# Kernel tuning notes

Measured on AMD Instinct MI355X. Metric: run time of the kernel, lower is better.

## Reference

```python
import jax, jax.numpy as jnp
import numpy as np

N = 524288          # query points
N_COMP = 36         # sdf_n_comp
GRID = 512          # cubic grid resolution
SDF_DIM = 256
APP_DIM = 128
MAT_MODE = [(0, 1), (0, 2), (1, 2)]
VEC_MODE = [2, 1, 0]
PE_FREQS = (1.0, 2.0, 4.0)  # sdf_multires=3, log-sampled 2^0..2^2


def _pos_enc(x):
    # NeRF embedder, include_input=True: [x, sin(f x), cos(f x) per freq]
    outs = [x]
    for f in PE_FREQS:
        outs.append(jnp.sin(x * f))
        outs.append(jnp.cos(x * f))
    return jnp.concatenate(outs, axis=-1)  # (N, 21)


def _bilinear_plane(plane, gx, gy):
    # plane: (C, H, W); gx indexes W, gy indexes H; align_corners=True
    C, H, W = plane.shape
    px = (gx + 1.0) * 0.5 * (W - 1)
    py = (gy + 1.0) * 0.5 * (H - 1)
    x0 = jnp.clip(jnp.floor(px), 0, W - 2).astype(jnp.int32)
    y0 = jnp.clip(jnp.floor(py), 0, H - 2).astype(jnp.int32)
    x1, y1 = x0 + 1, y0 + 1
    wx = px - x0
    wy = py - y0
    f00 = plane[:, y0, x0]  # (C, N)
    f01 = plane[:, y0, x1]
    f10 = plane[:, y1, x0]
    f11 = plane[:, y1, x1]
    return (f00 * (1 - wx) + f01 * wx) * (1 - wy) + (f10 * (1 - wx) + f11 * wx) * wy


def _linear_line(line, g):
    # line: (C, L); g in [-1, 1]; align_corners=True
    C, L = line.shape
    p = (g + 1.0) * 0.5 * (L - 1)
    i0 = jnp.clip(jnp.floor(p), 0, L - 2).astype(jnp.int32)
    w = p - i0
    return line[:, i0] * (1 - w) + line[:, i0 + 1] * w  # (C, N)


def setup_inputs() -> dict:
    key = jax.random.key(0)
    ks = jax.random.split(key, 6)
    xyz = jax.random.uniform(ks[0], (N, 3), dtype=jnp.float32)  # points in aabb [0,1]^3
    planes = jax.random.normal(ks[1], (3, N_COMP, GRID, GRID), dtype=jnp.float32) * 0.1
    lines = jax.random.normal(ks[2], (3, N_COMP, GRID), dtype=jnp.float32) * 0.1
    in_ch = N_COMP * 3 + 21  # 129
    W1 = jax.random.normal(ks[3], (in_ch, SDF_DIM), dtype=jnp.float32) * (np.sqrt(2.0) / np.sqrt(SDF_DIM))
    b1 = jnp.zeros((SDF_DIM,), dtype=jnp.float32)
    W2 = jax.random.normal(ks[4], (SDF_DIM, 1 + APP_DIM), dtype=jnp.float32) * 0.0001 + np.sqrt(np.pi) / np.sqrt(SDF_DIM)
    b2 = jnp.full((1 + APP_DIM,), -0.2, dtype=jnp.float32)  # init_radius bias
    return {"xyz": xyz, "planes": planes, "lines": lines, "W1": W1, "b1": b1, "W2": W2, "b2": b2}


def reference(xyz, planes, lines, W1, b1, W2, b2):
    # contraction: normalize aabb [0,1]^3 -> [-1,1]
    xn = 2.0 * xyz - 1.0  # (N, 3)
    # sampling coords are detached in the original (coordinate_plane.detach())
    xs = jax.lax.stop_gradient(xn)
    feats = []
    for i in range(3):
        m0, m1 = MAT_MODE[i]
        pfeat = _bilinear_plane(planes[i], xs[:, m0], xs[:, m1])  # (C, N)
        lfeat = _linear_line(lines[i], xs[:, VEC_MODE[i]])        # (C, N)
        feats.append(pfeat * lfeat)
    feat = jnp.concatenate(feats, axis=0).T  # (N, 3C)
    pe = _pos_enc(xn)                         # (N, 21)
    h = jnp.concatenate([feat, pe], axis=-1)  # (N, 129)
    h = jax.nn.softplus(100.0 * (h @ W1 + b1)) / 100.0  # Softplus(beta=100)
    out = h @ W2 + b2  # (N, 1 + app_dim); out[..., :1] is the SDF
    return out
```

## Files before the change

kernel.cpp:

```cpp
#include <hip/hip_runtime.h>
#include <math.h>

typedef unsigned short u16;
typedef unsigned int u32;
typedef __attribute__((ext_vector_type(8))) short short8;
typedef __attribute__((ext_vector_type(4))) float f32x4;

#define OFF_LINES_T 62914560u
#define OFF_W1S     63037440u
#define OFF_W2S     63119360u
#define WS_NEEDED   63217664u

__device__ __forceinline__ float bf_lo(u32 u){ union{u32 i;float f;} v; v.i = u << 16; return v.f; }
__device__ __forceinline__ float bf_hi(u32 u){ union{u32 i;float f;} v; v.i = u & 0xffff0000u; return v.f; }
__device__ __forceinline__ u16 f2bf(float f){ union{float f;u32 i;} v; v.f=f; u32 i=v.i; return (u16)((i + 0x7fffu + ((i>>16)&1u)) >> 16); }
__device__ __forceinline__ u32 pack2bf(float lo, float hi){ return (u32)f2bf(lo) | ((u32)f2bf(hi)<<16); }

__global__ void k_tp(const float* __restrict__ planes, u16* __restrict__ pt){
  int t = blockIdx.x*256 + threadIdx.x;
  int i = t >> 18;
  int yx = t & 262143;
  const float* src = planes + (size_t)i*9437184 + yx;
  uint4* dst = reinterpret_cast<uint4*>(pt + (size_t)t*40);
#pragma unroll
  for (int cc=0; cc<5; cc++){
    float v[8];
#pragma unroll
    for (int e=0;e<8;e++){
      int c = cc*8+e;
      v[e] = (c<36) ? src[(size_t)c*262144] : 0.f;
    }
    uint4 o; o.x=pack2bf(v[0],v[1]); o.y=pack2bf(v[2],v[3]); o.z=pack2bf(v[4],v[5]); o.w=pack2bf(v[6],v[7]);
    dst[cc]=o;
  }
}

__global__ void k_tl(const float* __restrict__ lines, u16* __restrict__ lt){
  int t = blockIdx.x*256 + threadIdx.x;
  int i = t >> 9, g = t & 511;
  const float* src = lines + (size_t)i*18432 + g;
  uint4* dst = reinterpret_cast<uint4*>(lt + (size_t)t*40);
#pragma unroll
  for (int cc=0; cc<5; cc++){
    float v[8];
#pragma unroll
    for (int e=0;e<8;e++){
      int c = cc*8+e;
      v[e] = (c<36) ? src[(size_t)c*512] : 0.f;
    }
    uint4 o; o.x=pack2bf(v[0],v[1]); o.y=pack2bf(v[2],v[3]); o.z=pack2bf(v[4],v[5]); o.w=pack2bf(v[6],v[7]);
    dst[cc]=o;
  }
}

__device__ __forceinline__ int map_k1(int kp){
  if (kp < 120){ int q = kp/40, r = kp - q*40; return (r<36) ? q*36 + r : -1; }
  if (kp < 141) return kp - 12;
  return -1;
}

__global__ void k_w1(const float* __restrict__ W1, u16* __restrict__ w1s){
  int t = blockIdx.x*256 + threadIdx.x;
  int lane = t & 63;
  int fid = t >> 6;
  int nt = fid/5, kt = fid - nt*5;
  int n = nt*16 + (lane & 15);
  int kb = kt*32 + (lane >> 4)*8;
  float v[8];
#pragma unroll
  for (int j=0;j<8;j++){ int k = map_k1(kb+j); v[j] = (k>=0) ? W1[k*256+n] : 0.f; }
  uint4 o; o.x=pack2bf(v[0],v[1]); o.y=pack2bf(v[2],v[3]); o.z=pack2bf(v[4],v[5]); o.w=pack2bf(v[6],v[7]);
  *reinterpret_cast<uint4*>(w1s + (size_t)t*8) = o;
}

__global__ void k_w2(const float* __restrict__ W2, u16* __restrict__ w2s){
  int t = blockIdx.x*256 + threadIdx.x;
  int lane = t & 63;
  int fid = t >> 6;
  int kb = (fid & 7)*32 + (lane >> 4)*8;
  int n = (fid >> 3)*16 + (lane & 15);
  float v[8];
#pragma unroll
  for (int j=0;j<8;j++){ int k = kb+j; v[j] = (n<129) ? W2[k*129+n] : 0.f; }
  uint4 o; o.x=pack2bf(v[0],v[1]); o.y=pack2bf(v[2],v[3]); o.z=pack2bf(v[4],v[5]); o.w=pack2bf(v[6],v[7]);
  *reinterpret_cast<uint4*>(w2s + (size_t)t*8) = o;
}

__device__ __forceinline__ u32 blend(u32 u00,u32 u01,u32 u10,u32 u11,u32 g0,u32 g1,
                                     float wx,float wy,float wz){
  float r[2];
#pragma unroll
  for (int h=0; h<2; h++){
    float f00 = h ? bf_hi(u00) : bf_lo(u00);
    float f01 = h ? bf_hi(u01) : bf_lo(u01);
    float f10 = h ? bf_hi(u10) : bf_lo(u10);
    float f11 = h ? bf_hi(u11) : bf_lo(u11);
    float e0  = h ? bf_hi(g0)  : bf_lo(g0);
    float e1  = h ? bf_hi(g1)  : bf_lo(g1);
    float a  = f00 + (f01-f00)*wx;
    float b  = f10 + (f11-f10)*wx;
    float pf = a + (b-a)*wy;
    float lf = e0 + (e1-e0)*wz;
    r[h] = pf*lf;
  }
  return pack2bf(r[0], r[1]);
}

#define FSTRIDE 168
#define HSTRIDE 264

__global__ void __launch_bounds__(256) k_main(
    const float* __restrict__ xyz, const u16* __restrict__ pt,
    const u16* __restrict__ lt, const u16* __restrict__ w1s,
    const u16* __restrict__ w2s, const float* __restrict__ b1,
    const float* __restrict__ b2, float* __restrict__ out)
{
  __shared__ u16 smem[64*HSTRIDE];
  const int tid = threadIdx.x;
  const int p = tid >> 2, q = tid & 3;
  const int gp = blockIdx.x*64 + p;
  const float u0 = xyz[gp*3], u1 = xyz[gp*3+1], u2 = xyz[gp*3+2];
  const float xn0 = 2.f*u0-1.f, xn1 = 2.f*u1-1.f, xn2 = 2.f*u2-1.f;

  if (q < 3){
    float gxv, gyv, gzv;
    if      (q==0){ gxv=xn0; gyv=xn1; gzv=xn2; }
    else if (q==1){ gxv=xn0; gyv=xn2; gzv=xn1; }
    else          { gxv=xn1; gyv=xn2; gzv=xn0; }
    float px=(gxv+1.0f)*0.5f*511.0f, py=(gyv+1.0f)*0.5f*511.0f, pz=(gzv+1.0f)*0.5f*511.0f;
    float fx=fminf(fmaxf(floorf(px),0.f),510.f);
    float fy=fminf(fmaxf(floorf(py),0.f),510.f);
    float fz=fminf(fmaxf(floorf(pz),0.f),510.f);
    int ix=(int)fx, iy=(int)fy, iz=(int)fz;
    float wx=px-fx, wy=py-fy, wz=pz-fz;
    const u16* base  = pt + (size_t)((q<<18)+(iy<<9)+ix)*40;
    const u16* lbase = lt + (size_t)((q<<9)+iz)*40;
    u16* dst = smem + p*FSTRIDE + q*40;
#pragma unroll
    for (int cc=0; cc<5; cc++){
      const uint4 a00 = *reinterpret_cast<const uint4*>(base + cc*8);
      const uint4 a01 = *reinterpret_cast<const uint4*>(base + 40 + cc*8);
      const uint4 a10 = *reinterpret_cast<const uint4*>(base + 20480 + cc*8);
      const uint4 a11 = *reinterpret_cast<const uint4*>(base + 20520 + cc*8);
      const uint4 e0  = *reinterpret_cast<const uint4*>(lbase + cc*8);
      const uint4 e1  = *reinterpret_cast<const uint4*>(lbase + 40 + cc*8);
      uint4 o;
      o.x = blend(a00.x,a01.x,a10.x,a11.x,e0.x,e1.x,wx,wy,wz);
      o.y = blend(a00.y,a01.y,a10.y,a11.y,e0.y,e1.y,wx,wy,wz);
      o.z = blend(a00.z,a01.z,a10.z,a11.z,e0.z,e1.z,wx,wy,wz);
      o.w = blend(a00.w,a01.w,a10.w,a11.w,e0.w,e1.w,wx,wy,wz);
      *reinterpret_cast<uint4*>(dst + cc*8) = o;
    }
  } else {
    float v[21];
    v[0]=xn0; v[1]=xn1; v[2]=xn2;
    v[3]=__sinf(xn0);      v[4]=__sinf(xn1);      v[5]=__sinf(xn2);
    v[6]=__cosf(xn0);      v[7]=__cosf(xn1);      v[8]=__cosf(xn2);
    v[9]=__sinf(2.f*xn0);  v[10]=__sinf(2.f*xn1); v[11]=__sinf(2.f*xn2);
    v[12]=__cosf(2.f*xn0); v[13]=__cosf(2.f*xn1); v[14]=__cosf(2.f*xn2);
    v[15]=__sinf(4.f*xn0); v[16]=__sinf(4.f*xn1); v[17]=__sinf(4.f*xn2);
    v[18]=__cosf(4.f*xn0); v[19]=__cosf(4.f*xn1); v[20]=__cosf(4.f*xn2);
    u16* dst = smem + p*FSTRIDE + 120;
#pragma unroll
    for (int cc=0; cc<5; cc++){
      float w0 = (cc*8+0<21)?v[cc*8+0]:0.f; float w1v=(cc*8+1<21)?v[cc*8+1]:0.f;
      float w2v= (cc*8+2<21)?v[cc*8+2]:0.f; float w3 =(cc*8+3<21)?v[cc*8+3]:0.f;
      float w4 = (cc*8+4<21)?v[cc*8+4]:0.f; float w5 =(cc*8+5<21)?v[cc*8+5]:0.f;
      float w6 = (cc*8+6<21)?v[cc*8+6]:0.f; float w7 =(cc*8+7<21)?v[cc*8+7]:0.f;
      uint4 o; o.x=pack2bf(w0,w1v); o.y=pack2bf(w2v,w3); o.z=pack2bf(w4,w5); o.w=pack2bf(w6,w7);
      *reinterpret_cast<uint4*>(dst + cc*8) = o;
    }
  }
  __syncthreads();

  const int lane = tid & 63;
  const int w = tid >> 6;
  const int lm = lane & 15;
  const int quad = lane >> 4;
  const f32x4 zero = {0.f,0.f,0.f,0.f};
  f32x4 acc1[4][4];
#pragma unroll
  for (int mt=0; mt<4; mt++)
#pragma unroll
    for (int nt=0; nt<4; nt++) acc1[mt][nt] = zero;

#pragma unroll
  for (int kt=0; kt<5; kt++){
    short8 a[4];
#pragma unroll
    for (int mt=0; mt<4; mt++)
      a[mt] = *reinterpret_cast<const short8*>(smem + (mt*16 + lm)*FSTRIDE + kt*32 + quad*8);
    short8 b[4];
#pragma unroll
    for (int nt=0; nt<4; nt++)
      b[nt] = *reinterpret_cast<const short8*>(w1s + (size_t)(((w*4+nt)*5 + kt)*64 + lane)*8);
#pragma unroll
    for (int mt=0; mt<4; mt++)
#pragma unroll
      for (int nt=0; nt<4; nt++)
        acc1[mt][nt] = __builtin_amdgcn_mfma_f32_16x16x32_bf16(a[mt], b[nt], acc1[mt][nt], 0,0,0);
  }
  __syncthreads();

#pragma unroll
  for (int nt=0; nt<4; nt++){
    int col = w*64 + nt*16 + lm;
    float bias = b1[col];
#pragma unroll
    for (int mt=0; mt<4; mt++){
#pragma unroll
      for (int r=0; r<4; r++){
        float xv = acc1[mt][nt][r] + bias;
        float z = 100.f*xv;
        float y = (z > 15.f) ? xv : __logf(1.f + __expf(z))*0.01f;
        int row = mt*16 + quad*4 + r;
        smem[row*HSTRIDE + col] = f2bf(y);
      }
    }
  }
  __syncthreads();

  f32x4 acc2[4][3];
#pragma unroll
  for (int mt=0; mt<4; mt++)
#pragma unroll
    for (int nt=0; nt<3; nt++) acc2[mt][nt] = zero;

#pragma unroll
  for (int kt=0; kt<8; kt++){
    short8 a[4];
#pragma unroll
    for (int mt=0; mt<4; mt++)
      a[mt] = *reinterpret_cast<const short8*>(smem + (mt*16 + lm)*HSTRIDE + kt*32 + quad*8);
    short8 b[3];
#pragma unroll
    for (int nt=0; nt<3; nt++){
      int ntg = w + nt*4;
      b[nt] = *reinterpret_cast<const short8*>(w2s + (size_t)((ntg*8 + kt)*64 + lane)*8);
    }
#pragma unroll
    for (int mt=0; mt<4; mt++)
#pragma unroll
      for (int nt=0; nt<3; nt++)
        acc2[mt][nt] = __builtin_amdgcn_mfma_f32_16x16x32_bf16(a[mt], b[nt], acc2[mt][nt], 0,0,0);
  }

#pragma unroll
  for (int nt=0; nt<3; nt++){
    int j = (w + nt*4)*16 + lm;
    if (j < 129){
      float bias = b2[j];
#pragma unroll
      for (int mt=0; mt<4; mt++){
#pragma unroll
        for (int r=0; r<4; r++){
          int row = mt*16 + quad*4 + r;
          out[(size_t)(blockIdx.x*64 + row)*129 + j] = acc2[mt][nt][r] + bias;
        }
      }
    }
  }
}

extern "C" void kernel_launch(void* const* d_in, const int* in_sizes, int n_in,
                              void* d_out, int out_size, void* d_ws, size_t ws_size,
                              hipStream_t stream) {
  const float* xyz    = (const float*)d_in[0];
  const float* planes = (const float*)d_in[1];
  const float* lines  = (const float*)d_in[2];
  const float* W1     = (const float*)d_in[3];
  const float* b1     = (const float*)d_in[4];
  const float* W2     = (const float*)d_in[5];
  const float* b2     = (const float*)d_in[6];
  if (ws_size < (size_t)WS_NEEDED) return;

  u16* pt  = (u16*)((char*)d_ws);
  u16* lt  = (u16*)((char*)d_ws + OFF_LINES_T);
  u16* w1s = (u16*)((char*)d_ws + OFF_W1S);
  u16* w2s = (u16*)((char*)d_ws + OFF_W2S);

  k_tp<<<3072, 256, 0, stream>>>(planes, pt);
  k_tl<<<6,    256, 0, stream>>>(lines,  lt);
  k_w1<<<20,   256, 0, stream>>>(W1, w1s);
  k_w2<<<24,   256, 0, stream>>>(W2, w2s);
  k_main<<<8192, 256, 0, stream>>>(xyz, pt, lt, w1s, w2s, b1, b2, (float*)d_out);
}
```

Before: 689.5 us.

## Double threads per block, split gather and MLP tiles across eight waves

k_main now runs 512 threads per block. Two threads share each plane's gather for a point, each taking half of the 40 channels with 8-byte loads, and the 8 waves split the MLP into 2 M-halves by 4 N-groups. Bf16 packing in the hot paths switches to a cheaper round-half-up conversion built on a byte-permute. The goal is more memory-level parallelism for the random gathers and lower per-thread register pressure, at the cost of narrower loads, redundant B-fragment loads across waves, and slightly different rounding.

```diff
diff --git a/kernel.cpp b/kernel.cpp
--- a/kernel.cpp
+++ b/kernel.cpp
@@ -3,6 +3,7 @@
 
 typedef unsigned short u16;
 typedef unsigned int u32;
+typedef __attribute__((ext_vector_type(2))) u32 u32x2;
 typedef __attribute__((ext_vector_type(8))) short short8;
 typedef __attribute__((ext_vector_type(4))) float f32x4;
 
@@ -15,6 +16,11 @@
 __device__ __forceinline__ float bf_hi(u32 u){ union{u32 i;float f;} v; v.i = u & 0xffff0000u; return v.f; }
 __device__ __forceinline__ u16 f2bf(float f){ union{float f;u32 i;} v; v.f=f; u32 i=v.i; return (u16)((i + 0x7fffu + ((i>>16)&1u)) >> 16); }
 __device__ __forceinline__ u32 pack2bf(float lo, float hi){ return (u32)f2bf(lo) | ((u32)f2bf(hi)<<16); }
+__device__ __forceinline__ u32 pack2bf_fast(float lo, float hi){
+  return __builtin_amdgcn_perm(__float_as_uint(hi) + 0x8000u,
+                               __float_as_uint(lo) + 0x8000u, 0x07060302u);
+}
+__device__ __forceinline__ u16 f2bf_fast(float f){ return (u16)((__float_as_uint(f) + 0x8000u) >> 16); }
 
 __global__ void k_tp(const float* __restrict__ planes, u16* __restrict__ pt){
   int t = blockIdx.x*256 + threadIdx.x;
@@ -54,7 +60,7 @@
 }
 
 __device__ __forceinline__ int map_k1(int kp){
-  if (kp < 120){ int q = kp/40, r = kp - q*40; return (r<36) ? q*36 + r : -1; }
+  if (kp < 120){ int g = kp/40, r = kp - g*40; return (r<36) ? g*36 + r : -1; }
   if (kp < 141) return kp - 12;
   return -1;
 }
@@ -103,13 +109,13 @@
     float lf = e0 + (e1-e0)*wz;
     r[h] = pf*lf;
   }
-  return pack2bf(r[0], r[1]);
+  return pack2bf_fast(r[0], r[1]);
 }
 
 #define FSTRIDE 168
 #define HSTRIDE 264
 
-__global__ void __launch_bounds__(256) k_main(
+__global__ void __launch_bounds__(512, 4) k_main(
     const float* __restrict__ xyz, const u16* __restrict__ pt,
     const u16* __restrict__ lt, const u16* __restrict__ w1s,
     const u16* __restrict__ w2s, const float* __restrict__ b1,
@@ -117,15 +123,16 @@
 {
   __shared__ u16 smem[64*HSTRIDE];
   const int tid = threadIdx.x;
-  const int p = tid >> 2, q = tid & 3;
+  const int p = tid >> 3, q = tid & 7;
   const int gp = blockIdx.x*64 + p;
   const float u0 = xyz[gp*3], u1 = xyz[gp*3+1], u2 = xyz[gp*3+2];
   const float xn0 = 2.f*u0-1.f, xn1 = 2.f*u1-1.f, xn2 = 2.f*u2-1.f;
 
-  if (q < 3){
+  if (q < 6){
+    const int i = q >> 1, part = q & 1;
     float gxv, gyv, gzv;
-    if      (q==0){ gxv=xn0; gyv=xn1; gzv=xn2; }
-    else if (q==1){ gxv=xn0; gyv=xn2; gzv=xn1; }
+    if      (i==0){ gxv=xn0; gyv=xn1; gzv=xn2; }
+    else if (i==1){ gxv=xn0; gyv=xn2; gzv=xn1; }
     else          { gxv=xn1; gyv=xn2; gzv=xn0; }
     float px=(gxv+1.0f)*0.5f*511.0f, py=(gyv+1.0f)*0.5f*511.0f, pz=(gzv+1.0f)*0.5f*511.0f;
     float fx=fminf(fmaxf(floorf(px),0.f),510.f);
@@ -133,25 +140,23 @@
     float fz=fminf(fmaxf(floorf(pz),0.f),510.f);
     int ix=(int)fx, iy=(int)fy, iz=(int)fz;
     float wx=px-fx, wy=py-fy, wz=pz-fz;
-    const u16* base  = pt + (size_t)((q<<18)+(iy<<9)+ix)*40;
-    const u16* lbase = lt + (size_t)((q<<9)+iz)*40;
-    u16* dst = smem + p*FSTRIDE + q*40;
-#pragma unroll
-    for (int cc=0; cc<5; cc++){
-      const uint4 a00 = *reinterpret_cast<const uint4*>(base + cc*8);
-      const uint4 a01 = *reinterpret_cast<const uint4*>(base + 40 + cc*8);
-      const uint4 a10 = *reinterpret_cast<const uint4*>(base + 20480 + cc*8);
-      const uint4 a11 = *reinterpret_cast<const uint4*>(base + 20520 + cc*8);
-      const uint4 e0  = *reinterpret_cast<const uint4*>(lbase + cc*8);
-      const uint4 e1  = *reinterpret_cast<const uint4*>(lbase + 40 + cc*8);
-      uint4 o;
+    const u16* base  = pt + (size_t)((i<<18)+(iy<<9)+ix)*40 + part*20;
+    const u16* lbase = lt + (size_t)((i<<9)+iz)*40 + part*20;
+    u16* dst = smem + p*FSTRIDE + i*40 + part*20;
+#pragma unroll
+    for (int c=0; c<5; c++){
+      u32x2 a00 = *reinterpret_cast<const u32x2*>(base + c*4);
+      u32x2 a01 = *reinterpret_cast<const u32x2*>(base + 40 + c*4);
+      u32x2 a10 = *reinterpret_cast<const u32x2*>(base + 20480 + c*4);
+      u32x2 a11 = *reinterpret_cast<const u32x2*>(base + 20520 + c*4);
+      u32x2 e0  = *reinterpret_cast<const u32x2*>(lbase + c*4);
+      u32x2 e1  = *reinterpret_cast<const u32x2*>(lbase + 40 + c*4);
+      u32x2 o;
       o.x = blend(a00.x,a01.x,a10.x,a11.x,e0.x,e1.x,wx,wy,wz);
       o.y = blend(a00.y,a01.y,a10.y,a11.y,e0.y,e1.y,wx,wy,wz);
-      o.z = blend(a00.z,a01.z,a10.z,a11.z,e0.z,e1.z,wx,wy,wz);
-      o.w = blend(a00.w,a01.w,a10.w,a11.w,e0.w,e1.w,wx,wy,wz);
-      *reinterpret_cast<uint4*>(dst + cc*8) = o;
-    }
-  } else {
+      *reinterpret_cast<u32x2*>(dst + c*4) = o;
+    }
+  } else if (q == 6){
     float v[21];
     v[0]=xn0; v[1]=xn1; v[2]=xn2;
     v[3]=__sinf(xn0);      v[4]=__sinf(xn1);      v[5]=__sinf(xn2);
@@ -162,40 +167,38 @@
     v[18]=__cosf(4.f*xn0); v[19]=__cosf(4.f*xn1); v[20]=__cosf(4.f*xn2);
     u16* dst = smem + p*FSTRIDE + 120;
 #pragma unroll
-    for (int cc=0; cc<5; cc++){
-      float w0 = (cc*8+0<21)?v[cc*8+0]:0.f; float w1v=(cc*8+1<21)?v[cc*8+1]:0.f;
-      float w2v= (cc*8+2<21)?v[cc*8+2]:0.f; float w3 =(cc*8+3<21)?v[cc*8+3]:0.f;
-      float w4 = (cc*8+4<21)?v[cc*8+4]:0.f; float w5 =(cc*8+5<21)?v[cc*8+5]:0.f;
-      float w6 = (cc*8+6<21)?v[cc*8+6]:0.f; float w7 =(cc*8+7<21)?v[cc*8+7]:0.f;
-      uint4 o; o.x=pack2bf(w0,w1v); o.y=pack2bf(w2v,w3); o.z=pack2bf(w4,w5); o.w=pack2bf(w6,w7);
-      *reinterpret_cast<uint4*>(dst + cc*8) = o;
+    for (int c=0; c<20; c++){
+      float a = (c*2  <21)?v[c*2  ]:0.f;
+      float b = (c*2+1<21)?v[c*2+1]:0.f;
+      *reinterpret_cast<u32*>(dst + c*2) = pack2bf_fast(a,b);
     }
   }
   __syncthreads();
 
   const int lane = tid & 63;
   const int w = tid >> 6;
+  const int wm = w & 1, wn = w >> 1;
   const int lm = lane & 15;
   const int quad = lane >> 4;
   const f32x4 zero = {0.f,0.f,0.f,0.f};
-  f32x4 acc1[4][4];
-#pragma unroll
-  for (int mt=0; mt<4; mt++)
+  f32x4 acc1[2][4];
+#pragma unroll
+  for (int mt=0; mt<2; mt++)
 #pragma unroll
     for (int nt=0; nt<4; nt++) acc1[mt][nt] = zero;
 
 #pragma unroll
   for (int kt=0; kt<5; kt++){
-    short8 a[4];
-#pragma unroll
-    for (int mt=0; mt<4; mt++)
-      a[mt] = *reinterpret_cast<const short8*>(smem + (mt*16 + lm)*FSTRIDE + kt*32 + quad*8);
+    short8 a[2];
+#pragma unroll
+    for (int mt=0; mt<2; mt++)
+      a[mt] = *reinterpret_cast<const short8*>(smem + ((wm*2+mt)*16 + lm)*FSTRIDE + kt*32 + quad*8);
     short8 b[4];
 #pragma unroll
     for (int nt=0; nt<4; nt++)
-      b[nt] = *reinterpret_cast<const short8*>(w1s + (size_t)(((w*4+nt)*5 + kt)*64 + lane)*8);
-#pragma unroll
-    for (int mt=0; mt<4; mt++)
+      b[nt] = *reinterpret_cast<const short8*>(w1s + (size_t)(((wn*4+nt)*5 + kt)*64 + lane)*8);
+#pragma unroll
+    for (int mt=0; mt<2; mt++)
 #pragma unroll
       for (int nt=0; nt<4; nt++)
         acc1[mt][nt] = __builtin_amdgcn_mfma_f32_16x16x32_bf16(a[mt], b[nt], acc1[mt][nt], 0,0,0);
@@ -204,42 +207,42 @@
 
 #pragma unroll
   for (int nt=0; nt<4; nt++){
-    int col = w*64 + nt*16 + lm;
+    int col = wn*64 + nt*16 + lm;
     float bias = b1[col];
 #pragma unroll
-    for (int mt=0; mt<4; mt++){
+    for (int mt=0; mt<2; mt++){
 #pragma unroll
       for (int r=0; r<4; r++){
         float xv = acc1[mt][nt][r] + bias;
         float z = 100.f*xv;
         float y = (z > 15.f) ? xv : __logf(1.f + __expf(z))*0.01f;
-        int row = mt*16 + quad*4 + r;
-        smem[row*HSTRIDE + col] = f2bf(y);
+        int row = (wm*2+mt)*16 + quad*4 + r;
+        smem[row*HSTRIDE + col] = f2bf_fast(y);
       }
     }
   }
   __syncthreads();
 
-  f32x4 acc2[4][3];
-#pragma unroll
-  for (int mt=0; mt<4; mt++)
+  f32x4 acc2[2][3];
+#pragma unroll
+  for (int mt=0; mt<2; mt++)
 #pragma unroll
     for (int nt=0; nt<3; nt++) acc2[mt][nt] = zero;
 
 #pragma unroll
   for (int kt=0; kt<8; kt++){
-    short8 a[4];
-#pragma unroll
-    for (int mt=0; mt<4; mt++)
-      a[mt] = *reinterpret_cast<const short8*>(smem + (mt*16 + lm)*HSTRIDE + kt*32 + quad*8);
+    short8 a[2];
+#pragma unroll
+    for (int mt=0; mt<2; mt++)
+      a[mt] = *reinterpret_cast<const short8*>(smem + ((wm*2+mt)*16 + lm)*HSTRIDE + kt*32 + quad*8);
     short8 b[3];
 #pragma unroll
     for (int nt=0; nt<3; nt++){
-      int ntg = w + nt*4;
+      int ntg = wn*3 + nt;
       b[nt] = *reinterpret_cast<const short8*>(w2s + (size_t)((ntg*8 + kt)*64 + lane)*8);
     }
 #pragma unroll
-    for (int mt=0; mt<4; mt++)
+    for (int mt=0; mt<2; mt++)
 #pragma unroll
       for (int nt=0; nt<3; nt++)
         acc2[mt][nt] = __builtin_amdgcn_mfma_f32_16x16x32_bf16(a[mt], b[nt], acc2[mt][nt], 0,0,0);
@@ -247,14 +250,14 @@
 
 #pragma unroll
   for (int nt=0; nt<3; nt++){
-    int j = (w + nt*4)*16 + lm;
+    int j = (wn*3 + nt)*16 + lm;
     if (j < 129){
       float bias = b2[j];
 #pragma unroll
-      for (int mt=0; mt<4; mt++){
+      for (int mt=0; mt<2; mt++){
 #pragma unroll
         for (int r=0; r<4; r++){
-          int row = mt*16 + quad*4 + r;
+          int row = (wm*2+mt)*16 + quad*4 + r;
           out[(size_t)(blockIdx.x*64 + row)*129 + j] = acc2[mt][nt][r] + bias;
         }
       }
@@ -283,5 +286,5 @@
   k_tl<<<6,    256, 0, stream>>>(lines,  lt);
   k_w1<<<20,   256, 0, stream>>>(W1, w1s);
   k_w2<<<24,   256, 0, stream>>>(W2, w2s);
-  k_main<<<8192, 256, 0, stream>>>(xyz, pt, lt, w1s, w2s, b1, b2, (float*)d_out);
-}
+  k_main<<<8192, 512, 0, stream>>>(xyz, pt, lt, w1s, w2s, b1, b2, (float*)d_out);
+}
```

Measured after the change: 656.1 us. 4.8% less time.
